# Optimization experiments

Hardware: AMD Instinct MI355X
Metric: run time of the kernel (lower is better)

Reference implementation:

```python
import jax, jax.numpy as jnp
import numpy as np

B, L, W, S, STEPS, VOCAB, NLAB = 1024, 128, 512, 8, 12, 32, 10

def setup_inputs() -> dict:
    key = jax.random.key(0)
    ks = jax.random.split(key, 24)
    def nrm(k, shape, scale=0.05):
        return jax.random.normal(k, shape, jnp.float32) * scale
    x = jax.random.randint(ks[0], (B, L), 0, VOCAB)
    embed = nrm(ks[1], (VOCAB, W), 0.1).at[0].set(0.0)  # padding_idx=0
    return {
        'x': x,
        'embed': embed,
        'W_mix': nrm(ks[2], (W, 3 * W)), 'b_mix': jnp.zeros((W,), jnp.float32),
        'W_in': nrm(ks[3], (S, W, 2 * W)), 'b_in': jnp.zeros((S, W), jnp.float32),
        'W_link': nrm(ks[4], (S, W, W)), 'b_link': jnp.zeros((S, W), jnp.float32),
        'W_ih': nrm(ks[5], (S, 3 * W, W)), 'b_ih': jnp.zeros((S, 3 * W), jnp.float32),
        'W_hh': nrm(ks[6], (S, 3 * W, W)), 'b_hh': jnp.zeros((S, 3 * W), jnp.float32),
        'W_gate': nrm(ks[7], (S, 1, W)), 'b_gate': jnp.zeros((S, 1), jnp.float32),
        'phase': nrm(ks[8], (S, W), 0.5), 'prism_gain': jnp.zeros((S, W), jnp.float32),
        'W_delta': nrm(ks[9], (S, W, W)), 'b_delta': jnp.zeros((S, W), jnp.float32),
        'decay_param': jnp.zeros((), jnp.float32),
        'W_out': nrm(ks[10], (NLAB, W)), 'b_out': jnp.zeros((NLAB,), jnp.float32),
    }

def _encode(x, embed, W_mix, b_mix):
    emb = embed[x]                                          # [B,L,W]
    mask = (x != 0).astype(jnp.float32)[..., None]          # [B,L,1]
    summed = (emb * mask).sum(1)
    denom = jnp.maximum(mask.sum(1), 1.0)
    mean = summed / denom
    maxed = jnp.where(mask == 0, -10000.0, emb).max(1)
    maxed = jnp.where(jnp.isfinite(maxed), maxed, 0.0)
    last_idx = jnp.maximum(mask[..., 0].sum(1).astype(jnp.int32) - 1, 0)
    last = jnp.take_along_axis(emb, last_idx[:, None, None], axis=1)[:, 0]
    cat = jnp.concatenate([mean, maxed, last], -1)          # [B,3W]
    return jnp.tanh(cat @ W_mix.T + b_mix)

def _forward(x, embed, W_mix, b_mix, W_in, b_in, W_link, b_link, W_ih, b_ih,
             W_hh, b_hh, W_gate, b_gate, phase, prism_gain, W_delta, b_delta,
             decay_param, W_out, b_out):
    summary = _encode(x, embed, W_mix, b_mix)               # [B,W]
    decay = jax.nn.sigmoid(decay_param)
    inv_sqrt_s = np.float32(1.0 / np.sqrt(S))
    gain = jax.nn.softplus(prism_gain)[None]                # [1,S,W]

    def step(carry, _):
        h, hs = carry
        shared = jnp.concatenate([h, summary], -1)          # conditioned: [B,2W]
        f0 = jnp.tanh(jnp.einsum('swi,bi->bsw', W_in, shared) + b_in)      # [B,S,W]
        prev = jnp.roll(f0, 1, axis=1)                      # sparse ring: feats[(i-1)%S]
        feats = jnp.tanh(f0 + jnp.einsum('sow,bsw->bso', W_link, prev) + b_link)
        # recurrent side pockets: per-side GRUCell (torch gate order r,z,n)
        gi = jnp.einsum('sgw,bsw->bsg', W_ih, feats) + b_ih
        gh = jnp.einsum('sgw,bsw->bsg', W_hh, hs) + b_hh
        ir, iz, inn = jnp.split(gi, 3, -1)
        hr, hz, hn = jnp.split(gh, 3, -1)
        r = jax.nn.sigmoid(ir + hr)
        z = jax.nn.sigmoid(iz + hz)
        n = jnp.tanh(inn + r * hn)
        hs_new = (1.0 - z) * n + z * hs                     # [B,S,W]
        feat = hs_new
        gate = jax.nn.sigmoid(jnp.einsum('sow,bsw->bso', W_gate, feat) + b_gate)  # [B,S,1]
        feat = jnp.cos(feat + phase[None]) ** 2 * gain      # prismion
        upd = gate * jnp.tanh(jnp.einsum('sow,bsw->bso', W_delta, feat) + b_delta)
        delta = upd.sum(1) * inv_sqrt_s
        h_new = jnp.tanh(h * decay + delta)
        return (h_new, hs_new), None

    hs0 = jnp.zeros((B, S, W), jnp.float32)
    (h, _), _ = jax.lax.scan(step, (summary, hs0), None, length=STEPS)
    return h @ W_out.T + b_out                               # [B,10]

def reference(x, embed, W_mix, b_mix, W_in, b_in, W_link, b_link, W_ih, b_ih,
              W_hh, b_hh, W_gate, b_gate, phase, prism_gain, W_delta, b_delta,
              decay_param, W_out, b_out):
    return _forward(x, embed, W_mix, b_mix, W_in, b_in, W_link, b_link, W_ih,
                    b_ih, W_hh, b_hh, W_gate, b_gate, phase, prism_gain,
                    W_delta, b_delta, decay_param, W_out, b_out)
```

## Files before the change

kernel.cpp:

```cpp
#include <hip/hip_runtime.h>
#include <hip/hip_bf16.h>


typedef unsigned short u16;
typedef __attribute__((ext_vector_type(8))) short short8;
typedef __attribute__((ext_vector_type(4))) float f32x4;

__device__ __forceinline__ float bf2f(u16 v) {
    union { unsigned int u; float f; } x; x.u = ((unsigned int)v) << 16; return x.f;
}
__device__ __forceinline__ u16 f2bf(float f) {
    union { float f; unsigned int u; } x; x.f = f;
    unsigned int u = x.u;
    return (u16)((u + 0x7FFFu + ((u >> 16) & 1u)) >> 16);
}
__device__ __forceinline__ float fsig(float v) {
    return __builtin_amdgcn_rcpf(1.f + __expf(-v));
}
__device__ __forceinline__ float ftanh(float v) {
    return 1.f - 2.f * __builtin_amdgcn_rcpf(__expf(2.f * v) + 1.f);
}
__device__ __forceinline__ float fsoftplus(float v) {
    return (v > 20.f) ? v : __logf(1.f + __expf(v));
}

union U4 { ushort4 v; u16 e[4]; };

__device__ __forceinline__ void gload_lds16(const u16* g, u16* l) {
    __builtin_amdgcn_global_load_lds(
        (const __attribute__((address_space(1))) unsigned int*)g,
        (__attribute__((address_space(3))) unsigned int*)l, 16, 0, 0);
}

__device__ __forceinline__ int sane16(u16 u) {
    if ((u & 0x7FFF) == 0) return 1;
    int e = (u >> 7) & 0xFF;
    return (e >= 0x33 && e <= 0x43) ? 1 : 0;
}
__global__ __launch_bounds__(256) void detect_k(const u16* __restrict__ raw,
                                                int* __restrict__ flag) {
    const int t = threadIdx.x;
    int c = sane16(raw[1024 + t * 2]) + sane16(raw[1024 + t * 2 + 1]);
#pragma unroll
    for (int off = 32; off; off >>= 1) c += __shfl_down(c, off, 64);
    __shared__ int red[4];
    if ((t & 63) == 0) red[t >> 6] = c;
    __syncthreads();
    if (t == 0) *flag = (red[0] + red[1] + red[2] + red[3] >= 448) ? 1 : 0;
}

struct CT { const void* src[20]; int n[20]; int off[20]; };
__global__ __launch_bounds__(256) void conv_k(CT ct, u16* __restrict__ dstBase,
                                              const int* __restrict__ flag) {
    const int isbf = *flag;
    const int gid = blockIdx.x * 256 + threadIdx.x;
    const int stride = gridDim.x * 256;
    for (int tn = 0; tn < 20; ++tn) {
        const int n = ct.n[tn];
        const int n4 = n >> 2;
        u16* dst = dstBase + ct.off[tn];
        if (!isbf) {
            const float* s = (const float*)ct.src[tn];
            for (int i = gid; i < n4; i += stride) {
                f32x4 v = *(const f32x4*)(s + i * 4);
                *(ushort4*)(dst + i * 4) =
                    make_ushort4(f2bf(v[0]), f2bf(v[1]), f2bf(v[2]), f2bf(v[3]));
            }
            if (gid < (n & 3)) { int i = n4 * 4 + gid; dst[i] = f2bf(s[i]); }
        } else {
            const u16* s = (const u16*)ct.src[tn];
            for (int i = gid; i < n4; i += stride)
                *(ushort4*)(dst + i * 4) = *(const ushort4*)(s + i * 4);
            if (gid < (n & 3)) { int i = n4 * 4 + gid; dst[i] = s[i]; }
        }
    }
}

__global__ __launch_bounds__(256) void pack_k(const u16* __restrict__ Wih,
                                              const u16* __restrict__ Whh,
                                              u16* __restrict__ Wcat) {
    long i = ((long)blockIdx.x * 256 + threadIdx.x) * 8;
    if (i >= 8L * 1536 * 512) return;
    long sg = i >> 9;
    long k  = i & 511;
    *(short8*)(Wcat + sg * 1024 + k)       = *(const short8*)(Wih + i);
    *(short8*)(Wcat + sg * 1024 + 512 + k) = *(const short8*)(Whh + i);
}

struct GP {
    const u16* A;  long lda; long aOff[8];
    const u16* Bw; long ldb; long bwOff[8];
    const u16* bias; long biasOff[8];
    const u16* add; long ldadd; long addOff;
    const float* gate_pre;
    const u16* bgate;
    void* C; long ldc; long cOff[8];
    float* C2;
    u16* C3;
    int K; int nt;
};

template<int EPI, int MT, int SWZ, int PIPE, int NK>
__global__ __launch_bounds__(256) void gemm_k(GP p) {
    constexpr int MW   = MT / 32;
    constexpr int AITS = MT / 32;
    constexpr int NBUF = PIPE ? 3 : 2;
    __shared__ __align__(16) u16 lA[NBUF][MT * 64];
    __shared__ __align__(16) u16 lB[NBUF][128 * 64];
    const int t    = threadIdx.x;
    const int lane = t & 63;
    const int wv   = t >> 6;
    int bx = blockIdx.x, byy = blockIdx.y;
    if (SWZ) {
        int wgid = bx + (byy << 5);
        bx  = ((wgid & 7) << 2) + ((wgid >> 3) & 3);
        byy = wgid >> 5;
    }
    const int z    = bx / p.nt;
    const int n0   = (bx - z * p.nt) * 128;
    const int m0   = byy * MT;

    const u16* Ab = p.A + p.aOff[z] + (long)m0 * p.lda;
    const u16* Bb = p.Bw + p.bwOff[z] + (long)n0 * p.ldb;

    f32x4 acc[MW][4];
#pragma unroll
    for (int i = 0; i < MW; i++)
#pragma unroll
        for (int j = 0; j < 4; j++) acc[i][j] = (f32x4){0.f, 0.f, 0.f, 0.f};

    const int wm   = (wv & 1) * (MT / 2);
    const int wn   = (wv >> 1) * 64;
    const int fr   = lane & 15;
    const int quad = lane >> 4;

    auto stage = [&](int buf, long kb) {
#pragma unroll
        for (int it = 0; it < AITS; ++it) {
            int flat = it * 256 + t, row = flat >> 3, src = (flat & 7) ^ (row & 7);
            gload_lds16(Ab + (long)row * p.lda + kb + src * 8, &lA[buf][flat * 8]);
        }
#pragma unroll
        for (int it = 0; it < 4; ++it) {
            int flat = it * 256 + t, row = flat >> 3, src = (flat & 7) ^ (row & 7);
            gload_lds16(Bb + (long)row * p.ldb + kb + src * 8, &lB[buf][flat * 8]);
        }
    };
    auto inner = [&](int cur) {
#pragma unroll
        for (int kk = 0; kk < 2; ++kk) {
            const int q = kk * 4 + quad;
            short8 aF[MW], bF[4];
#pragma unroll
            for (int mi = 0; mi < MW; mi++) {
                int row = wm + mi * 16 + fr;
                aF[mi] = *(const short8*)&lA[cur][row * 64 + (q ^ (row & 7)) * 8];
            }
#pragma unroll
            for (int ni = 0; ni < 4; ni++) {
                int row = wn + ni * 16 + fr;
                bF[ni] = *(const short8*)&lB[cur][row * 64 + (q ^ (row & 7)) * 8];
            }
#pragma unroll
            for (int mi = 0; mi < MW; mi++)
#pragma unroll
                for (int ni = 0; ni < 4; ni++)
                    acc[mi][ni] = __builtin_amdgcn_mfma_f32_16x16x32_bf16(
                        aF[mi], bF[ni], acc[mi][ni], 0, 0, 0);
        }
    };

    if (PIPE == 0) {
        const int nk = p.K >> 6;
        stage(0, 0);
        __syncthreads();
        for (int kt = 0; kt < nk; ++kt) {
            const int cur = kt & 1, nxt = cur ^ 1;
            if (kt + 1 < nk) stage(nxt, (long)(kt + 1) * 64);
            inner(cur);
            __syncthreads();
        }
    } else {
        stage(0, 0); stage(1, 64);
        asm volatile("s_waitcnt vmcnt(6)" ::: "memory");
        __builtin_amdgcn_s_barrier();
#pragma unroll
        for (int kt = 0; kt < NK; ++kt) {
            if (kt + 2 < NK) stage((kt + 2) % 3, (long)(kt + 2) * 64);
            inner(kt % 3);
            if (kt + 1 < NK) {
                if (kt + 2 < NK)
                    asm volatile("s_waitcnt vmcnt(6) lgkmcnt(0)" ::: "memory");
                else
                    asm volatile("s_waitcnt vmcnt(0) lgkmcnt(0)" ::: "memory");
                __builtin_amdgcn_s_barrier();
            }
        }
    }

    float sgv[MW][4];
    if (EPI == 3) {
#pragma unroll
        for (int mi = 0; mi < MW; mi++)
#pragma unroll
            for (int r = 0; r < 4; r++) {
                long row = m0 + wm + mi * 16 + quad * 4 + r;
                sgv[mi][r] = fsig(p.gate_pre[row * 8 + z] + bf2f(p.bgate[z]));
            }
    }

#pragma unroll
    for (int mi = 0; mi < MW; mi++) {
#pragma unroll
        for (int ni = 0; ni < 4; ni++) {
            const int mg = m0 + wm + mi * 16 + quad * 4;
            const int ng = n0 + wn + ni * 16 + fr;
#pragma unroll
            for (int r = 0; r < 4; r++) {
                float v = acc[mi][ni][r];
                const long row = mg + r;
                if (EPI == 1) {
                    float ad = bf2f(p.add[z * p.addOff + row * p.ldadd + ng]);
                    v = ftanh(v + ad + bf2f(p.bias[p.biasOff[z] + ng]));
                    ((u16*)p.C)[p.cOff[z] + row * p.ldc + ng] = f2bf(v);
                } else if (EPI == 3) {
                    v = ftanh(v + bf2f(p.bias[p.biasOff[z] + ng])) * sgv[mi][r];
                    ((u16*)p.C)[p.cOff[z] + row * p.ldc + ng] = f2bf(v);
                } else if (EPI == 4) {
                    v = ftanh(v + bf2f(p.bias[ng]));
                    u16 b = f2bf(v);
                    ((u16*)p.C)[row * 512 + ng] = b;
                    p.C3[row * 512 + ng] = b;
                    p.C2[row * 512 + ng] = v;
                } else if (EPI == 6) {
                    v = v + bf2f(p.bias[p.biasOff[z] + ng]);
                    ((u16*)p.C)[p.cOff[z] + row * p.ldc + ng] = f2bf(v);
                } else {
                    float ad = bf2f(p.add[row * p.ldadd + ng]);
                    v = ftanh(v + ad);
                    ((u16*)p.C)[row * p.ldc + ng] = f2bf(v);
                }
            }
        }
    }
}

struct GGP {
    const u16* fhs_in;
    u16* fhs_out;
    const u16* Wcat;
    const u16* b_ih;
    const u16* b_hh;
    u16* prism;
    float* gate_pre;
    const u16* Wg;
    const u16* phase;
    const u16* pgain;
};

__global__ __launch_bounds__(256, 2) void grug_k(GGP p) {
    __shared__ __align__(16) u16 sA[2][64 * 32];
    __shared__ __align__(16) u16 sW[2][3][128 * 32];
    const int t    = threadIdx.x;
    const int lane = t & 63;
    const int wv   = t >> 6;
    const int wgid = blockIdx.x + (blockIdx.y << 5);
    const int s    = wgid & 7;
    const int idx  = wgid >> 3;
    const int w0   = (idx & 3) * 128;
    const int m0   = (idx >> 2) * 64;
    const int fr   = lane & 15;
    const int quad = lane >> 4;
    const int wn   = wv * 32;

    const u16* Ab = p.fhs_in + (long)m0 * 8192 + s * 1024;
    const u16* Wb = p.Wcat + (long)s * 1536 * 1024;

    f32x4 acc[4][4][2];
#pragma unroll
    for (int q = 0; q < 4; q++)
#pragma unroll
        for (int mi = 0; mi < 4; mi++)
#pragma unroll
            for (int ni = 0; ni < 2; ni++) acc[q][mi][ni] = (f32x4){0.f,0.f,0.f,0.f};

    const int arow = t >> 2, ac4 = t & 3, asrc = ac4 ^ ((arow >> 1) & 3);

    auto stageA = [&](int buf, long kb) {
        gload_lds16(Ab + (long)arow * 8192 + kb + asrc * 8, &sA[buf][t * 8]);
    };
    auto stageW = [&](int buf, long kb) {
#pragma unroll
        for (int q = 0; q < 3; q++)
#pragma unroll
            for (int it = 0; it < 2; ++it) {
                int flat = it * 256 + t, row = flat >> 2, src = (flat & 3) ^ ((row >> 1) & 3);
                long g = (long)(q * 512 + w0 + row);
                gload_lds16(Wb + g * 1024 + kb + src * 8, &sW[buf][q][flat * 8]);
            }
    };

    stageA(0, 0); stageW(0, 0);
    __syncthreads();

    for (int kt = 0; kt < 32; ++kt) {
        const int cur = kt & 1, nxt = cur ^ 1;
        if (kt + 1 < 32) { stageA(nxt, (long)(kt + 1) * 32); stageW(nxt, (long)(kt + 1) * 32); }
        const int qsel = (kt < 16) ? 2 : 3;
        short8 aF[4], bF[3][2];
#pragma unroll
        for (int mi = 0; mi < 4; mi++) {
            int row = mi * 16 + fr;
            aF[mi] = *(const short8*)&sA[cur][row * 32 + ((quad ^ ((row >> 1) & 3)) & 3) * 8];
        }
#pragma unroll
        for (int q = 0; q < 3; q++)
#pragma unroll
            for (int ni = 0; ni < 2; ni++) {
                int row = wn + ni * 16 + fr;
                bF[q][ni] = *(const short8*)&sW[cur][q][row * 32 + ((quad ^ ((row >> 1) & 3)) & 3) * 8];
            }
#pragma unroll
        for (int mi = 0; mi < 4; mi++)
#pragma unroll
            for (int ni = 0; ni < 2; ni++) {
                acc[0][mi][ni] = __builtin_amdgcn_mfma_f32_16x16x32_bf16(aF[mi], bF[0][ni], acc[0][mi][ni], 0, 0, 0);
                acc[1][mi][ni] = __builtin_amdgcn_mfma_f32_16x16x32_bf16(aF[mi], bF[1][ni], acc[1][mi][ni], 0, 0, 0);
                if (qsel == 2)
                    acc[2][mi][ni] = __builtin_amdgcn_mfma_f32_16x16x32_bf16(aF[mi], bF[2][ni], acc[2][mi][ni], 0, 0, 0);
                else
                    acc[3][mi][ni] = __builtin_amdgcn_mfma_f32_16x16x32_bf16(aF[mi], bF[2][ni], acc[3][mi][ni], 0, 0, 0);
            }
        __syncthreads();
    }

    const u16* bih = p.b_ih + (long)s * 1536;
    const u16* bhh = p.b_hh + (long)s * 1536;
    float gp[4][4];
#pragma unroll
    for (int mi = 0; mi < 4; mi++)
#pragma unroll
        for (int r = 0; r < 4; r++) gp[mi][r] = 0.f;

#pragma unroll
    for (int ni = 0; ni < 2; ni++) {
        const int col = w0 + wn + ni * 16 + fr;
        const float br  = bf2f(bih[col])        + bf2f(bhh[col]);
        const float bz  = bf2f(bih[512 + col])  + bf2f(bhh[512 + col]);
        const float bin = bf2f(bih[1024 + col]);
        const float bhn = bf2f(bhh[1024 + col]);
        const float ph  = bf2f(p.phase[s * 512 + col]);
        const float gain = fsoftplus(bf2f(p.pgain[s * 512 + col]));
        const float wg  = bf2f(p.Wg[s * 512 + col]);
#pragma unroll
        for (int mi = 0; mi < 4; mi++) {
#pragma unroll
            for (int r = 0; r < 4; r++) {
                const long b = m0 + mi * 16 + quad * 4 + r;
                float rv = fsig(acc[0][mi][ni][r] + br);
                float zv = fsig(acc[1][mi][ni][r] + bz);
                float nv = ftanh(acc[2][mi][ni][r] + bin + rv * (acc[3][mi][ni][r] + bhn));
                float hold = bf2f(p.fhs_in[b * 8192 + s * 1024 + 512 + col]);
                float hv = (1.f - zv) * nv + zv * hold;
                p.fhs_out[b * 8192 + s * 1024 + 512 + col] = f2bf(hv);
                float c = __cosf(hv + ph);
                p.prism[b * 4096 + s * 512 + col] = f2bf(c * c * gain);
                gp[mi][r] += wg * hv;
            }
        }
    }
#pragma unroll
    for (int m = 1; m < 16; m <<= 1)
#pragma unroll
        for (int mi = 0; mi < 4; mi++)
#pragma unroll
            for (int r = 0; r < 4; r++) gp[mi][r] += __shfl_xor(gp[mi][r], m, 64);
    if (fr == 0) {
#pragma unroll
        for (int mi = 0; mi < 4; mi++)
#pragma unroll
            for (int r = 0; r < 4; r++) {
                long b = m0 + mi * 16 + quad * 4 + r;
                atomicAdd(&p.gate_pre[b * 8 + s], gp[mi][r]);
            }
    }
}

__global__ __launch_bounds__(256) void encode_k(const int* __restrict__ x,
                                                const u16* __restrict__ embed,
                                                u16* __restrict__ cat) {
    __shared__ int toks[128];
    __shared__ int cnt_s;
    const int b = blockIdx.x, t = threadIdx.x;
    if (t < 128) toks[t] = x[b * 128 + t];
    __syncthreads();
    if (t == 0) {
        int c = 0;
        for (int l = 0; l < 128; l++) c += (toks[l] != 0);
        cnt_s = c;
    }
    __syncthreads();
    const int cnt = cnt_s;
    const int lastTok = toks[cnt > 0 ? cnt - 1 : 0];
    for (int w = t; w < 512; w += 256) {
        float sum = 0.f, mx = -10000.f;
        for (int l = 0; l < 128; l++) {
            int tok = toks[l];
            if (tok != 0) {
                float e = bf2f(embed[tok * 512 + w]);
                sum += e;
                mx = fmaxf(mx, e);
            }
        }
        float mean = sum / (float)(cnt > 0 ? cnt : 1);
        float last = bf2f(embed[lastTok * 512 + w]);
        cat[(long)b * 1536 + w]        = f2bf(mean);
        cat[(long)b * 1536 + 512 + w]  = f2bf(mx);
        cat[(long)b * 1536 + 1024 + w] = f2bf(last);
    }
}

__global__ __launch_bounds__(256) void hupd_k(const u16* __restrict__ upd,
                                              float* __restrict__ h,
                                              u16* __restrict__ h_b,
                                              const u16* __restrict__ decay_p,
                                              float* __restrict__ gate_pre) {
    const int idx = blockIdx.x * 256 + threadIdx.x;
    if (idx < 8192) gate_pre[idx] = 0.f;
    const int b = idx >> 9, w = idx & 511;
    const long base = (long)b * 4096 + w;
    float dsum = 0.f;
#pragma unroll
    for (int s = 0; s < 8; s++) dsum += bf2f(upd[base + s * 512]);
    const float decay = fsig(bf2f(decay_p[0]));
    const float hv = ftanh(h[idx] * decay + dsum * 0.35355339059327373f);
    h[idx] = hv;
    h_b[idx] = f2bf(hv);
}

__global__ __launch_bounds__(64) void out_k(const float* __restrict__ h,
                                            const u16* __restrict__ Wout,
                                            const u16* __restrict__ bout,
                                            void* __restrict__ out,
                                            const int* __restrict__ flag) {
    const int b = blockIdx.x, lane = threadIdx.x;
    const int isbf = *flag;
    for (int j = 0; j < 10; j++) {
        float p = 0.f;
#pragma unroll
        for (int k = 0; k < 8; k++) {
            int w = lane + k * 64;
            p += h[(long)b * 512 + w] * bf2f(Wout[j * 512 + w]);
        }
#pragma unroll
        for (int off = 32; off; off >>= 1) p += __shfl_down(p, off, 64);
        if (lane == 0) {
            float val = p + bf2f(bout[j]);
            if (isbf) ((u16*)out)[b * 10 + j] = f2bf(val);
            else      ((float*)out)[b * 10 + j] = val;
        }
    }
}

extern "C" void kernel_launch(void* const* d_in, const int* in_sizes, int n_in,
                              void* d_out, int out_size, void* d_ws, size_t ws_size,
                              hipStream_t stream) {
    (void)n_in; (void)out_size; (void)ws_size;
    const int* x = (const int*)d_in[0];

    char* pp = (char*)d_ws;
    auto carve = [&](size_t n) { char* r = pp; pp += (n + 255) & ~(size_t)255; return (void*)r; };

    CT ct;
    size_t ctot = 0;
    for (int i = 0; i < 20; i++) {
        ct.src[i] = d_in[i + 1];
        ct.n[i]   = in_sizes[i + 1];
        ct.off[i] = (int)ctot;
        ctot += ((size_t)in_sizes[i + 1] + 15) & ~(size_t)15;
    }
    u16* canon = (u16*)carve(ctot * 2);
    const u16* embed  = canon + ct.off[0];
    const u16* W_mix  = canon + ct.off[1];
    const u16* b_mix  = canon + ct.off[2];
    const u16* W_in   = canon + ct.off[3];
    const u16* b_in   = canon + ct.off[4];
    const u16* W_link = canon + ct.off[5];
    const u16* b_link = canon + ct.off[6];
    const u16* W_ih   = canon + ct.off[7];
    const u16* b_ih   = canon + ct.off[8];
    const u16* W_hh   = canon + ct.off[9];
    const u16* b_hh   = canon + ct.off[10];
    const u16* W_gate = canon + ct.off[11];
    const u16* b_gate = canon + ct.off[12];
    const u16* phase  = canon + ct.off[13];
    const u16* pgain  = canon + ct.off[14];
    const u16* W_delta= canon + ct.off[15];
    const u16* b_delta= canon + ct.off[16];
    const u16* decayp = canon + ct.off[17];
    const u16* W_out  = canon + ct.off[18];
    const u16* b_out  = canon + ct.off[19];

    int*   flag   = (int*)  carve(256);
    u16*   Wcat   = (u16*)  carve((size_t)8 * 1536 * 1024 * 2);
    u16*   cat    = (u16*)  carve((size_t)1024 * 1536 * 2);
    u16*   h_b    = (u16*)  carve((size_t)1024 * 512 * 2);
    u16*   summ_b = (u16*)  carve((size_t)1024 * 512 * 2);
    float* h      = (float*)carve((size_t)1024 * 512 * 4);
    u16*   cin    = (u16*)  carve((size_t)1024 * 4096 * 2);
    u16*   f0     = (u16*)  carve((size_t)1024 * 4096 * 2);
    u16*   fhs0   = (u16*)  carve((size_t)1024 * 8192 * 2);
    u16*   fhs1   = (u16*)  carve((size_t)1024 * 8192 * 2);
    u16*   prism  = (u16*)  carve((size_t)1024 * 4096 * 2);
    u16*   upd    = (u16*)  carve((size_t)1024 * 4096 * 2);
    float* gate_pre = (float*)carve((size_t)1024 * 8 * 4);

    (void)hipMemsetAsync(fhs0, 0, (size_t)1024 * 8192 * 2, stream);
    (void)hipMemsetAsync(fhs1, 0, (size_t)1024 * 8192 * 2, stream);
    (void)hipMemsetAsync(gate_pre, 0, (size_t)1024 * 8 * 4, stream);

    detect_k<<<dim3(1), dim3(256), 0, stream>>>((const u16*)d_in[1], flag);
    conv_k<<<dim3(1024), dim3(256), 0, stream>>>(ct, canon, flag);
    pack_k<<<dim3(3072), dim3(256), 0, stream>>>(W_ih, W_hh, Wcat);
    encode_k<<<dim3(1024), dim3(256), 0, stream>>>(x, embed, cat);

    {
        GP p{}; p.A = cat; p.lda = 1536; p.Bw = W_mix; p.ldb = 1536;
        p.bias = b_mix; p.C = h_b; p.ldc = 512; p.C2 = h; p.C3 = summ_b;
        p.K = 1536; p.nt = 4;
        gemm_k<4, 64, 0, 0, 0><<<dim3(4, 16, 1), dim3(256), 0, stream>>>(p);
    }
    {
        GP p{}; p.A = summ_b; p.lda = 512; p.Bw = W_in + 512; p.ldb = 1024;
        p.bias = b_in; p.C = cin; p.ldc = 4096; p.K = 512; p.nt = 32;
        gemm_k<6, 64, 1, 1, 8><<<dim3(32, 16, 1), dim3(256), 0, stream>>>(p);
    }

    for (int step = 0; step < 12; ++step) {
        u16* fhs_cur = (step & 1) ? fhs1 : fhs0;
        u16* fhs_nxt = (step & 1) ? fhs0 : fhs1;
        {
            GP p{}; p.A = h_b; p.lda = 512; p.Bw = W_in; p.ldb = 1024;
            p.add = cin; p.ldadd = 4096; p.C = f0; p.ldc = 4096;
            p.K = 512; p.nt = 32;
            gemm_k<7, 64, 1, 1, 8><<<dim3(32, 16, 1), dim3(256), 0, stream>>>(p);
        }
        {
            GP p{}; p.A = f0; p.lda = 4096;
            for (int s = 0; s < 8; s++) p.aOff[s] = (long)((s + 7) & 7) * 512;
            p.Bw = W_link; p.ldb = 512;
            for (int s = 0; s < 8; s++) p.bwOff[s] = (long)s * 512 * 512;
            p.bias = b_link;
            for (int s = 0; s < 8; s++) p.biasOff[s] = (long)s * 512;
            p.add = f0; p.ldadd = 4096; p.addOff = 512;
            p.C = fhs_cur; p.ldc = 8192;
            for (int s = 0; s < 8; s++) p.cOff[s] = (long)s * 1024;
            p.K = 512; p.nt = 4;
            gemm_k<1, 64, 1, 1, 8><<<dim3(32, 16, 1), dim3(256), 0, stream>>>(p);
        }
        {
            GGP g{};
            g.fhs_in = fhs_cur; g.fhs_out = fhs_nxt; g.Wcat = Wcat;
            g.b_ih = b_ih; g.b_hh = b_hh; g.prism = prism; g.gate_pre = gate_pre;
            g.Wg = W_gate; g.phase = phase; g.pgain = pgain;
            grug_k<<<dim3(32, 16, 1), dim3(256), 0, stream>>>(g);
        }
        {
            GP p{}; p.A = prism; p.lda = 4096;
            for (int s = 0; s < 8; s++) p.aOff[s] = (long)s * 512;
            p.Bw = W_delta; p.ldb = 512;
            for (int s = 0; s < 8; s++) p.bwOff[s] = (long)s * 512 * 512;
            p.bias = b_delta;
            for (int s = 0; s < 8; s++) p.biasOff[s] = (long)s * 512;
            p.gate_pre = gate_pre; p.bgate = b_gate;
            p.C = upd; p.ldc = 4096;
            for (int s = 0; s < 8; s++) p.cOff[s] = (long)s * 512;
            p.K = 512; p.nt = 4;
            gemm_k<3, 64, 1, 1, 8><<<dim3(32, 16, 1), dim3(256), 0, stream>>>(p);
        }
        hupd_k<<<dim3(2048), dim3(256), 0, stream>>>(upd, h, h_b, decayp, gate_pre);
    }

    out_k<<<dim3(1024), dim3(64), 0, stream>>>(h, W_out, b_out, d_out, flag);
}
```

Baseline: 1.534 ms.

## Enlarge GRU GEMM tile to 128x128 with triple-buffered weights and interleaved staging

The fused GRU gate kernel now uses 512 threads per block covering 128 batch rows instead of 64, so each staged weight tile is reused across twice as many rows and the grid is halved. Weight tiles are triple-buffered and issued two k-steps ahead, with the loads split per gate and interleaved between three MFMA phases. Explicit waitcnt, barriers and setprio replace the single syncthreads. LDS use grows to about 80 KB per block, and launch_bounds(512,2) may add register pressure and lower occupancy.

```diff
diff --git a/kernel.cpp b/kernel.cpp
--- a/kernel.cpp
+++ b/kernel.cpp
@@ -258,9 +258,9 @@
     const u16* pgain;
 };
 
-__global__ __launch_bounds__(256, 2) void grug_k(GGP p) {
-    __shared__ __align__(16) u16 sA[2][64 * 32];
-    __shared__ __align__(16) u16 sW[2][3][128 * 32];
+__global__ __launch_bounds__(512, 2) void grug_k(GGP p) {
+    __shared__ __align__(16) u16 sA[2][128 * 32];
+    __shared__ __align__(16) u16 sW[3][3][128 * 32];
     const int t    = threadIdx.x;
     const int lane = t & 63;
     const int wv   = t >> 6;
@@ -268,12 +268,13 @@
     const int s    = wgid & 7;
     const int idx  = wgid >> 3;
     const int w0   = (idx & 3) * 128;
-    const int m0   = (idx >> 2) * 64;
+    const int m0   = (idx >> 2) * 128;
     const int fr   = lane & 15;
     const int quad = lane >> 4;
-    const int wn   = wv * 32;
-
-    const u16* Ab = p.fhs_in + (long)m0 * 8192 + s * 1024;
+    const int wm   = (wv & 1) * 64;
+    const int wn   = (wv >> 1) * 32;
+
+    const u16* Ab = p.fhs_in + (long)m0 * 8192 + (long)s * 1024;
     const u16* Wb = p.Wcat + (long)s * 1536 * 1024;
 
     f32x4 acc[4][4][2];
@@ -286,52 +287,94 @@
 
     const int arow = t >> 2, ac4 = t & 3, asrc = ac4 ^ ((arow >> 1) & 3);
 
-    auto stageA = [&](int buf, long kb) {
-        gload_lds16(Ab + (long)arow * 8192 + kb + asrc * 8, &sA[buf][t * 8]);
+    auto stageA = [&](int buf, int kt) {
+        gload_lds16(Ab + (long)arow * 8192 + kt * 32 + asrc * 8, &sA[buf][t * 8]);
     };
-    auto stageW = [&](int buf, long kb) {
-#pragma unroll
-        for (int q = 0; q < 3; q++)
-#pragma unroll
-            for (int it = 0; it < 2; ++it) {
-                int flat = it * 256 + t, row = flat >> 2, src = (flat & 3) ^ ((row >> 1) & 3);
-                long g = (long)(q * 512 + w0 + row);
-                gload_lds16(Wb + g * 1024 + kb + src * 8, &sW[buf][q][flat * 8]);
-            }
+    auto stageWq = [&](int buf, int kt, int q) {
+        long g = (long)(q * 512 + w0 + arow);
+        gload_lds16(Wb + g * 1024 + kt * 32 + asrc * 8, &sW[buf][q][t * 8]);
     };
 
-    stageA(0, 0); stageW(0, 0);
-    __syncthreads();
-
+    stageA(0, 0);
+    stageWq(0, 0, 0); stageWq(0, 0, 1); stageWq(0, 0, 2);
+    stageWq(1, 1, 0); stageWq(1, 1, 1); stageWq(1, 1, 2);
+    asm volatile("s_waitcnt vmcnt(3)" ::: "memory");
+    __builtin_amdgcn_s_barrier();
+
+    int aCur = 0, wCur = 0;
     for (int kt = 0; kt < 32; ++kt) {
-        const int cur = kt & 1, nxt = cur ^ 1;
-        if (kt + 1 < 32) { stageA(nxt, (long)(kt + 1) * 32); stageW(nxt, (long)(kt + 1) * 32); }
-        const int qsel = (kt < 16) ? 2 : 3;
-        short8 aF[4], bF[3][2];
+        const int aNxt = aCur ^ 1;
+        int wNx2 = wCur + 2; if (wNx2 >= 3) wNx2 -= 3;
+        short8 aF[4], bF0[2], bF1[2], bF2[2];
+
 #pragma unroll
         for (int mi = 0; mi < 4; mi++) {
-            int row = mi * 16 + fr;
-            aF[mi] = *(const short8*)&sA[cur][row * 32 + ((quad ^ ((row >> 1) & 3)) & 3) * 8];
-        }
-#pragma unroll
-        for (int q = 0; q < 3; q++)
-#pragma unroll
-            for (int ni = 0; ni < 2; ni++) {
-                int row = wn + ni * 16 + fr;
-                bF[q][ni] = *(const short8*)&sW[cur][q][row * 32 + ((quad ^ ((row >> 1) & 3)) & 3) * 8];
-            }
+            int row = wm + mi * 16 + fr;
+            aF[mi] = *(const short8*)&sA[aCur][row * 32 + ((quad ^ ((row >> 1) & 3)) & 3) * 8];
+        }
+#pragma unroll
+        for (int ni = 0; ni < 2; ni++) {
+            int row = wn + ni * 16 + fr;
+            bF0[ni] = *(const short8*)&sW[wCur][0][row * 32 + ((quad ^ ((row >> 1) & 3)) & 3) * 8];
+        }
+        if (kt + 1 < 32) stageA(aNxt, kt + 1);
+        if (kt + 2 < 32) stageWq(wNx2, kt + 2, 0);
+        __builtin_amdgcn_s_barrier();
+        asm volatile("s_waitcnt lgkmcnt(0)" ::: "memory");
+        __builtin_amdgcn_s_setprio(1);
 #pragma unroll
         for (int mi = 0; mi < 4; mi++)
 #pragma unroll
-            for (int ni = 0; ni < 2; ni++) {
-                acc[0][mi][ni] = __builtin_amdgcn_mfma_f32_16x16x32_bf16(aF[mi], bF[0][ni], acc[0][mi][ni], 0, 0, 0);
-                acc[1][mi][ni] = __builtin_amdgcn_mfma_f32_16x16x32_bf16(aF[mi], bF[1][ni], acc[1][mi][ni], 0, 0, 0);
-                if (qsel == 2)
-                    acc[2][mi][ni] = __builtin_amdgcn_mfma_f32_16x16x32_bf16(aF[mi], bF[2][ni], acc[2][mi][ni], 0, 0, 0);
-                else
-                    acc[3][mi][ni] = __builtin_amdgcn_mfma_f32_16x16x32_bf16(aF[mi], bF[2][ni], acc[3][mi][ni], 0, 0, 0);
-            }
-        __syncthreads();
+            for (int ni = 0; ni < 2; ni++)
+                acc[0][mi][ni] = __builtin_amdgcn_mfma_f32_16x16x32_bf16(aF[mi], bF0[ni], acc[0][mi][ni], 0, 0, 0);
+        __builtin_amdgcn_s_setprio(0);
+        __builtin_amdgcn_s_barrier();
+
+#pragma unroll
+        for (int ni = 0; ni < 2; ni++) {
+            int row = wn + ni * 16 + fr;
+            bF1[ni] = *(const short8*)&sW[wCur][1][row * 32 + ((quad ^ ((row >> 1) & 3)) & 3) * 8];
+        }
+        if (kt + 2 < 32) stageWq(wNx2, kt + 2, 1);
+        __builtin_amdgcn_s_barrier();
+        asm volatile("s_waitcnt lgkmcnt(0)" ::: "memory");
+        __builtin_amdgcn_s_setprio(1);
+#pragma unroll
+        for (int mi = 0; mi < 4; mi++)
+#pragma unroll
+            for (int ni = 0; ni < 2; ni++)
+                acc[1][mi][ni] = __builtin_amdgcn_mfma_f32_16x16x32_bf16(aF[mi], bF1[ni], acc[1][mi][ni], 0, 0, 0);
+        __builtin_amdgcn_s_setprio(0);
+        __builtin_amdgcn_s_barrier();
+
+#pragma unroll
+        for (int ni = 0; ni < 2; ni++) {
+            int row = wn + ni * 16 + fr;
+            bF2[ni] = *(const short8*)&sW[wCur][2][row * 32 + ((quad ^ ((row >> 1) & 3)) & 3) * 8];
+        }
+        if (kt + 2 < 32) stageWq(wNx2, kt + 2, 2);
+        if (kt < 30)       asm volatile("s_waitcnt vmcnt(3) lgkmcnt(0)" ::: "memory");
+        else if (kt == 30) asm volatile("s_waitcnt vmcnt(0) lgkmcnt(0)" ::: "memory");
+        else               asm volatile("s_waitcnt lgkmcnt(0)" ::: "memory");
+        __builtin_amdgcn_s_setprio(1);
+        if (kt < 16) {
+#pragma unroll
+            for (int mi = 0; mi < 4; mi++)
+#pragma unroll
+                for (int ni = 0; ni < 2; ni++)
+                    acc[2][mi][ni] = __builtin_amdgcn_mfma_f32_16x16x32_bf16(aF[mi], bF2[ni], acc[2][mi][ni], 0, 0, 0);
+        } else {
+#pragma unroll
+            for (int mi = 0; mi < 4; mi++)
+#pragma unroll
+                for (int ni = 0; ni < 2; ni++)
+                    acc[3][mi][ni] = __builtin_amdgcn_mfma_f32_16x16x32_bf16(aF[mi], bF2[ni], acc[3][mi][ni], 0, 0, 0);
+        }
+        __builtin_amdgcn_s_setprio(0);
+        __builtin_amdgcn_s_barrier();
+
+        aCur = aNxt;
+        wCur += 1; if (wCur >= 3) wCur -= 3;
     }
 
     const u16* bih = p.b_ih + (long)s * 1536;
@@ -356,7 +399,7 @@
         for (int mi = 0; mi < 4; mi++) {
 #pragma unroll
             for (int r = 0; r < 4; r++) {
-                const long b = m0 + mi * 16 + quad * 4 + r;
+                const long b = m0 + wm + mi * 16 + quad * 4 + r;
                 float rv = fsig(acc[0][mi][ni][r] + br);
                 float zv = fsig(acc[1][mi][ni][r] + bz);
                 float nv = ftanh(acc[2][mi][ni][r] + bin + rv * (acc[3][mi][ni][r] + bhn));
@@ -380,7 +423,7 @@
         for (int mi = 0; mi < 4; mi++)
 #pragma unroll
             for (int r = 0; r < 4; r++) {
-                long b = m0 + mi * 16 + quad * 4 + r;
+                long b = m0 + wm + mi * 16 + quad * 4 + r;
                 atomicAdd(&p.gate_pre[b * 8 + s], gp[mi][r]);
             }
     }
@@ -563,7 +606,7 @@
             g.fhs_in = fhs_cur; g.fhs_out = fhs_nxt; g.Wcat = Wcat;
             g.b_ih = b_ih; g.b_hh = b_hh; g.prism = prism; g.gate_pre = gate_pre;
             g.Wg = W_gate; g.phase = phase; g.pgain = pgain;
-            grug_k<<<dim3(32, 16, 1), dim3(256), 0, stream>>>(g);
+            grug_k<<<dim3(32, 8, 1), dim3(512), 0, stream>>>(g);
         }
         {
             GP p{}; p.A = prism; p.lda = 4096;
```

After: 1.499 ms. -2.3%, faster.
